# Kernel tuning notes

Measured on AMD Instinct MI355X. Metric: run time of the kernel, lower is better.

Reference implementation:

```python
import jax, jax.numpy as jnp
import numpy as np

N_USER, N_ITEM, D, K, E = 80000, 40000, 128, 10, 2000000

def _mlp(x, w1, b1, w2, b2, w3, b3):
    # MLP from source: linear->tanh->linear->tanh->linear->L2 normalize (eval mode, dropout off)
    x = jnp.tanh(x @ w1 + b1)
    x = jnp.tanh(x @ w2 + b2)
    x = x @ w3 + b3
    return x / jnp.maximum(jnp.linalg.norm(x, axis=-1, keepdims=True), 1e-12)

def setup_inputs() -> dict:
    key = jax.random.key(0)
    ks = jax.random.split(key, 24)
    s = 0.05
    inp = {
        'uemb_s': jax.random.normal(ks[0], (N_USER, D), jnp.float32),
        'iemb_s': jax.random.normal(ks[1], (N_ITEM, D), jnp.float32),
        'uemb_t': jax.random.normal(ks[2], (N_USER, D), jnp.float32),
        'u_emb_sp': jax.random.normal(ks[3], (N_USER, D), jnp.float32),
        'edge_user': jax.random.randint(ks[4], (E,), 0, N_USER, jnp.int32),
        'edge_item': jax.random.randint(ks[5], (E,), 0, N_ITEM, jnp.int32),
        # meta nets
        'Wu': jax.random.normal(ks[6], (4 * D, D), jnp.float32) * s,
        'bu': jnp.zeros((D,), jnp.float32),
        'Wi': jax.random.normal(ks[7], (2 * D, D), jnp.float32) * s,
        'bi': jnp.zeros((D,), jnp.float32),
        # mlp1: D -> D*K -> D//2 -> D*K
        'm1w1': jax.random.normal(ks[8], (D, D * K), jnp.float32) * s,
        'm1b1': jnp.zeros((D * K,), jnp.float32),
        'm1w2': jax.random.normal(ks[9], (D * K, D // 2), jnp.float32) * s,
        'm1b2': jnp.zeros((D // 2,), jnp.float32),
        'm1w3': jax.random.normal(ks[10], (D // 2, D * K), jnp.float32) * s,
        'm1b3': jnp.zeros((D * K,), jnp.float32),
        # mlp2: D -> D*K -> D//2 -> D*K
        'm2w1': jax.random.normal(ks[11], (D, D * K), jnp.float32) * s,
        'm2b1': jnp.zeros((D * K,), jnp.float32),
        'm2w2': jax.random.normal(ks[12], (D * K, D // 2), jnp.float32) * s,
        'm2b2': jnp.zeros((D // 2,), jnp.float32),
        'm2w3': jax.random.normal(ks[13], (D // 2, D * K), jnp.float32) * s,
        'm2b3': jnp.zeros((D * K,), jnp.float32),
    }
    return inp

def reference(uemb_s, iemb_s, uemb_t, u_emb_sp, edge_user, edge_item,
              Wu, bu, Wi, bi,
              m1w1, m1b1, m1w2, m1b2, m1w3, m1b3,
              m2w1, m2b1, m2w2, m2b2, m2w3, m2b3):
    # spmm with all-ones values == gather + segment_sum over the bipartite edge list
    neighbors_u = jax.ops.segment_sum(iemb_s[edge_item], edge_user, num_segments=N_USER)  # [U, D]
    tmp_embu = jax.lax.stop_gradient(
        jnp.concatenate([uemb_s, uemb_t, u_emb_sp, neighbors_u], axis=1)) @ Wu + bu       # [U, D]
    neighbors_i = jax.ops.segment_sum(((uemb_s + u_emb_sp) * 0.5)[edge_user], edge_item,
                                      num_segments=N_ITEM)                               # [I, D]
    tmp_embi = jax.lax.stop_gradient(
        jnp.concatenate([iemb_s, neighbors_i], axis=1)) @ Wi + bi                         # [I, D]
    metau = _mlp(tmp_embu, m1w1, m1b1, m1w2, m1b2, m1w3, m1b3).reshape(-1, D, K)          # [U, D, K]
    metai = _mlp(tmp_embi, m2w1, m2b1, m2w2, m2b2, m2w3, m2b3).reshape(-1, K, D)          # [I, K, D]
    meta_biasu = jnp.mean(metau, axis=0)  # [D, K]
    meta_biasi = jnp.mean(metai, axis=0)  # [K, D]
    low_weightu = jax.nn.softmax(metau + meta_biasu, axis=1)
    low_weighti = jax.nn.softmax(metai + meta_biasi, axis=1)
    return (low_weightu, low_weighti)
```

## Files before the change

### kernel.cpp

```cpp
#include <hip/hip_runtime.h>
#include <hip/hip_bf16.h>

#define D_ 128
#define DK_ 1280
#define K_ 10

typedef __attribute__((ext_vector_type(8))) short bh8;
typedef __attribute__((ext_vector_type(4))) short bh4;
typedef __attribute__((ext_vector_type(4))) float f32x4;

__device__ __forceinline__ short f2b(float f) {
    unsigned u = __builtin_bit_cast(unsigned, f);
    u += 0x7fffu + ((u >> 16) & 1u);
    return (short)(u >> 16);
}
__device__ __forceinline__ float b2f(short s) {
    unsigned u = ((unsigned)(unsigned short)s) << 16;
    return __builtin_bit_cast(float, u);
}
__device__ __forceinline__ float tanh_fast(float x) {
    float e = __expf(2.f * x);
    return 1.f - __fdividef(2.f, e + 1.f);
}
__device__ __forceinline__ f32x4 mfma16(bh8 a, bh8 b, f32x4 c) {
    return __builtin_amdgcn_mfma_f32_16x16x32_bf16(a, b, c, 0, 0, 0);
}

__device__ __forceinline__ int blk_excl_scan(int v, int t) {
    __shared__ int wp[4];
    int lane = t & 63, w = t >> 6;
    int s = v;
    for (int o = 1; o < 64; o <<= 1) {
        int pv = __shfl_up(s, o);
        if (lane >= o) s += pv;
    }
    if (lane == 63) wp[w] = s;
    __syncthreads();
    if (t == 0) {
        int a = 0;
#pragma unroll
        for (int k = 0; k < 4; ++k) { int x = wp[k]; wp[k] = a; a += x; }
    }
    __syncthreads();
    int r = s - v + wp[w];
    __syncthreads();
    return r;
}

__global__ __launch_bounds__(256) void cvt_all(
    const float* __restrict__ us, const float* __restrict__ ut,
    const float* __restrict__ usp, const float* __restrict__ is_,
    short* __restrict__ usb, short* __restrict__ utb,
    short* __restrict__ uspb, short* __restrict__ uavg, short* __restrict__ isb,
    int n4u, int n4i)
{
    int i = blockIdx.x * 256 + threadIdx.x;
    if (i < n4u) {
        float4 a = ((const float4*)us)[i];
        float4 b = ((const float4*)ut)[i];
        float4 c = ((const float4*)usp)[i];
        bh4 sa, sb, sc, sv;
        sa[0] = f2b(a.x); sa[1] = f2b(a.y); sa[2] = f2b(a.z); sa[3] = f2b(a.w);
        sb[0] = f2b(b.x); sb[1] = f2b(b.y); sb[2] = f2b(b.z); sb[3] = f2b(b.w);
        sc[0] = f2b(c.x); sc[1] = f2b(c.y); sc[2] = f2b(c.z); sc[3] = f2b(c.w);
        sv[0] = f2b(0.5f * (a.x + c.x)); sv[1] = f2b(0.5f * (a.y + c.y));
        sv[2] = f2b(0.5f * (a.z + c.z)); sv[3] = f2b(0.5f * (a.w + c.w));
        ((bh4*)usb)[i] = sa; ((bh4*)utb)[i] = sb;
        ((bh4*)uspb)[i] = sc; ((bh4*)uavg)[i] = sv;
    } else if (i < n4u + n4i) {
        int j = i - n4u;
        float4 v = ((const float4*)is_)[j];
        bh4 s;
        s[0] = f2b(v.x); s[1] = f2b(v.y); s[2] = f2b(v.z); s[3] = f2b(v.w);
        ((bh4*)isb)[j] = s;
    }
}

struct PackArgs {
    const float* W[8];
    short* o[8];
    int K[8];
    int N[8];
};
__global__ __launch_bounds__(256) void pack_all(PackArgs pa)
{
    int seg = blockIdx.y;
    int K = pa.K[seg], N = pa.N[seg];
    int total = K * N;
    int o = blockIdx.x * 256 + threadIdx.x;
    if (o >= total) return;
    const float* W = pa.W[seg];
    short* out = pa.o[seg];
    int j    = o & 7;
    int lane = (o >> 3) & 63;
    int rest = o >> 9;
    int KK = K >> 5;
    int kk = rest % KK;
    int tile = rest / KK;
    int k = kk * 32 + (lane >> 4) * 8 + j;
    int n = tile * 16 + (lane & 15);
    out[o] = f2b(W[(size_t)k * N + n]);
}

__global__ __launch_bounds__(256) void bhist_kernel(
    const int* __restrict__ eu, const int* __restrict__ ei,
    int* __restrict__ bcu, int* __restrict__ bci,
    int E, int shu, int shi, int nbu, int nbi)
{
    __shared__ int hu[160], hi[160];
    int t = threadIdx.x;
    int base = blockIdx.x * 4096;
    if (t < 160) { hu[t] = 0; hi[t] = 0; }
    __syncthreads();
    int n = min(4096, E - base);
#pragma unroll 4
    for (int k = 0; k < 16; ++k) {
        int idx = k * 256 + t;
        if (idx < n) {
            atomicAdd(&hu[eu[base + idx] >> shu], 1);
            atomicAdd(&hi[ei[base + idx] >> shi], 1);
        }
    }
    __syncthreads();
    if (t < nbu && hu[t]) atomicAdd(&bcu[t], hu[t]);
    if (t < nbi && hi[t]) atomicAdd(&bci[t], hi[t]);
}

__global__ __launch_bounds__(256) void binit_kernel(
    const int* __restrict__ bcu, int* __restrict__ gcu, int* __restrict__ bbu, int nbu,
    const int* __restrict__ bci, int* __restrict__ gci, int* __restrict__ bbi, int nbi,
    int E)
{
    int t = threadIdx.x;
    {
        int v = (t < nbu) ? bcu[t] : 0;
        int ex = blk_excl_scan(v, t);
        if (t < nbu) { gcu[t] = ex; bbu[t] = ex; }
        if (t == 0) bbu[nbu] = E;
    }
    __syncthreads();
    {
        int v = (t < nbi) ? bci[t] : 0;
        int ex = blk_excl_scan(v, t);
        if (t < nbi) { gci[t] = ex; bbi[t] = ex; }
        if (t == 0) bbi[nbi] = E;
    }
}

__global__ __launch_bounds__(256) void partition_kernel(
    const int* __restrict__ eu, const int* __restrict__ ei,
    int* __restrict__ gcu, int* __restrict__ gci,
    uint2* __restrict__ ebu, uint2* __restrict__ ebi,
    int E, int shu, int shi, int nbu, int nbi)
{
    __shared__ int hu[160], hi[160];
    int t = threadIdx.x;
    int base = blockIdx.x * 4096;
    if (t < 160) { hu[t] = 0; hi[t] = 0; }
    __syncthreads();
    int n = min(4096, E - base);
    int us[16], is_[16];
#pragma unroll 4
    for (int k = 0; k < 16; ++k) {
        int idx = k * 256 + t;
        if (idx < n) {
            us[k] = eu[base + idx];
            is_[k] = ei[base + idx];
            atomicAdd(&hu[us[k] >> shu], 1);
            atomicAdd(&hi[is_[k] >> shi], 1);
        } else us[k] = -1;
    }
    __syncthreads();
    if (t < nbu) { int c = hu[t]; hu[t] = c ? atomicAdd(&gcu[t], c) : 0; }
    if (t < nbi) { int c = hi[t]; hi[t] = c ? atomicAdd(&gci[t], c) : 0; }
    __syncthreads();
#pragma unroll 4
    for (int k = 0; k < 16; ++k) {
        if (us[k] >= 0) {
            int p1 = atomicAdd(&hu[us[k] >> shu], 1);
            ebu[p1] = make_uint2((unsigned)us[k], (unsigned)is_[k]);
            int p2 = atomicAdd(&hi[is_[k] >> shi], 1);
            ebi[p2] = make_uint2((unsigned)is_[k], (unsigned)us[k]);
        }
    }
}

__global__ __launch_bounds__(256) void fill2_all(
    const uint2* __restrict__ ebu, const int* __restrict__ bbu,
    int* __restrict__ off_u, int* __restrict__ end_u, int* __restrict__ adj_u,
    int NBU, int U,
    const uint2* __restrict__ ebi, const int* __restrict__ bbi,
    int* __restrict__ off_i, int* __restrict__ end_i, int* __restrict__ adj_i, int I)
{
    __shared__ int lcnt[512];
    __shared__ int lcur[512];
    bool isU = (int)blockIdx.x < NBU;
    const uint2* ebuf = isU ? ebu : ebi;
    const int* bbase  = isU ? bbu : bbi;
    int* off  = isU ? off_u : off_i;
    int* end_ = isU ? end_u : end_i;
    int* adj  = isU ? adj_u : adj_i;
    int span_sh = isU ? 9 : 8;
    int nrows = isU ? U : I;
    int b = isU ? blockIdx.x : blockIdx.x - NBU;

    int t = threadIdx.x;
    int rbase = b << span_sh;
    int span = min(1 << span_sh, nrows - rbase);
    int regbeg = bbase[b], regend = bbase[b + 1];
    for (int j = t; j < span; j += 256) lcnt[j] = 0;
    __syncthreads();
    for (int e = regbeg + t; e < regend; e += 256)
        atomicAdd(&lcnt[ebuf[e].x - rbase], 1);
    __syncthreads();
    int c0 = (2 * t < span) ? lcnt[2 * t] : 0;
    int c1 = (2 * t + 1 < span) ? lcnt[2 * t + 1] : 0;
    int ex = blk_excl_scan(c0 + c1, t);
    if (2 * t < span) {
        int beg = regbeg + ex;
        off[rbase + 2 * t] = beg;
        end_[rbase + 2 * t] = beg + c0;
        lcur[2 * t] = beg;
    }
    if (2 * t + 1 < span) {
        int beg = regbeg + ex + c0;
        off[rbase + 2 * t + 1] = beg;
        end_[rbase + 2 * t + 1] = beg + c1;
        lcur[2 * t + 1] = beg;
    }
    __syncthreads();
    for (int e = regbeg + t; e < regend; e += 256) {
        uint2 p = ebuf[e];
        int slot = atomicAdd(&lcur[p.x - rbase], 1);
        adj[slot] = (int)p.y;
    }
}

__global__ __launch_bounds__(256) void gather_all(
    const short* __restrict__ embU, const short* __restrict__ embI,
    const int* __restrict__ off_u, const int* __restrict__ end_u, const int* __restrict__ adj_u,
    const int* __restrict__ off_i, const int* __restrict__ end_i, const int* __restrict__ adj_i,
    short* __restrict__ nub, short* __restrict__ nib, int U, int I)
{
    int gw = (blockIdx.x * 256 + threadIdx.x) >> 6;
    int lane = threadIdx.x & 63;
    const short* emb; const int *offp, *endp, *adjp; short* outp; int row;
    if (gw < U)          { emb = embU; offp = off_u; endp = end_u; adjp = adj_u; outp = nub; row = gw; }
    else if (gw < U + I) { emb = embI; offp = off_i; endp = end_i; adjp = adj_i; outp = nib; row = gw - U; }
    else return;

    int beg = offp[row], end = endp[row];
    float ax = 0.f, ay = 0.f;
    int j = beg;
    for (; j + 3 < end; j += 4) {
        unsigned a = *(const unsigned*)(emb + (size_t)adjp[j]     * D_ + lane * 2);
        unsigned b = *(const unsigned*)(emb + (size_t)adjp[j + 1] * D_ + lane * 2);
        unsigned c = *(const unsigned*)(emb + (size_t)adjp[j + 2] * D_ + lane * 2);
        unsigned d = *(const unsigned*)(emb + (size_t)adjp[j + 3] * D_ + lane * 2);
        ax += b2f((short)(a & 0xffff)) + b2f((short)(b & 0xffff))
            + b2f((short)(c & 0xffff)) + b2f((short)(d & 0xffff));
        ay += b2f((short)(a >> 16)) + b2f((short)(b >> 16))
            + b2f((short)(c >> 16)) + b2f((short)(d >> 16));
    }
    for (; j < end; ++j) {
        unsigned a = *(const unsigned*)(emb + (size_t)adjp[j] * D_ + lane * 2);
        ax += b2f((short)(a & 0xffff));
        ay += b2f((short)(a >> 16));
    }
    unsigned o = ((unsigned)(unsigned short)f2b(ay) << 16) | (unsigned short)(unsigned)f2b(ax);
    *(unsigned*)(outp + (size_t)row * D_ + lane * 2) = o;
}

struct MlpArgs {
    const short *uA0, *uA1, *uA2, *uA3;
    const short *iA0, *iA1;
    const short *uWg, *uW1, *uW2, *uW3;
    const short *iWg, *iW1, *iW2, *iW3;
    const float *ubg, *ub1, *ub2, *ub3;
    const float *ibg, *ib1, *ib2, *ib3;
    short *uY, *iY;
    float *uNrm, *iNrm;
    int UB;
};

__global__ __launch_bounds__(256, 4) void fused_mlp_all(MlpArgs P)
{
    __shared__ char pool[35328];
    short* x2   = (short*)pool;
    short* h1q  = (short*)(pool + 8704);
    short* h2   = (short*)(pool + 29696);
    float* wred = (float*)(pool + 34304);

    const int t = threadIdx.x;
    const int l = t & 63;
    const int w = t >> 6;
    const int lr = l & 15;
    const int lg = l >> 4;

    const bool isU = (int)blockIdx.x < P.UB;
    const int bid = isU ? (int)blockIdx.x : (int)blockIdx.x - P.UB;
    const size_t rb0 = (size_t)bid * 32;
    const int KKG  = isU ? 16 : 8;
    const short* Wg = isU ? P.uWg : P.iWg;
    const short* W1 = isU ? P.uW1 : P.iW1;
    const short* W2 = isU ? P.uW2 : P.iW2;
    const short* W3 = isU ? P.uW3 : P.iW3;
    const float* bg = isU ? P.ubg : P.ibg;
    const float* b1 = isU ? P.ub1 : P.ib1;
    const float* b2 = isU ? P.ub2 : P.ib2;
    const float* b3 = isU ? P.ub3 : P.ib3;
    short* Ybf = isU ? P.uY : P.iY;
    float* Nrm = isU ? P.uNrm : P.iNrm;
    const short* srcs[4];
    if (isU) { srcs[0] = P.uA0; srcs[1] = P.uA1; srcs[2] = P.uA2; srcs[3] = P.uA3; }
    else     { srcs[0] = P.iA0; srcs[1] = P.iA1; srcs[2] = P.iA0; srcs[3] = P.iA1; }

    {
        f32x4 acc[2][2] = {{{0,0,0,0},{0,0,0,0}},{{0,0,0,0},{0,0,0,0}}};
        const short* wp = Wg + (size_t)(2 * w) * KKG * 512 + l * 8;
        const short* wq = wp + (size_t)KKG * 512;
        for (int kk = 0; kk < KKG; ++kk) {
            const short* src = srcs[kk >> 2];
            int coff = (kk & 3) * 32 + lg * 8;
            bh8 x0 = *(const bh8*)(src + (rb0 + lr) * D_ + coff);
            bh8 x1 = *(const bh8*)(src + (rb0 + 16 + lr) * D_ + coff);
            bh8 w0 = *(const bh8*)wp; wp += 512;
            bh8 w1 = *(const bh8*)wq; wq += 512;
            acc[0][0] = mfma16(w0, x0, acc[0][0]);
            acc[1][0] = mfma16(w0, x1, acc[1][0]);
            acc[0][1] = mfma16(w1, x0, acc[0][1]);
            acc[1][1] = mfma16(w1, x1, acc[1][1]);
        }
        float4 c0 = *(const float4*)(bg + (2 * w) * 16 + lg * 4);
        float4 c1 = *(const float4*)(bg + (2 * w + 1) * 16 + lg * 4);
#pragma unroll
        for (int rg = 0; rg < 2; ++rg) {
            bh4 p0, p1;
            p0[0] = f2b(acc[rg][0][0] + c0.x); p0[1] = f2b(acc[rg][0][1] + c0.y);
            p0[2] = f2b(acc[rg][0][2] + c0.z); p0[3] = f2b(acc[rg][0][3] + c0.w);
            p1[0] = f2b(acc[rg][1][0] + c1.x); p1[1] = f2b(acc[rg][1][1] + c1.y);
            p1[2] = f2b(acc[rg][1][2] + c1.z); p1[3] = f2b(acc[rg][1][3] + c1.w);
            *(bh4*)(x2 + (rg * 16 + lr) * 136 + (2 * w) * 16 + lg * 4) = p0;
            *(bh4*)(x2 + (rg * 16 + lr) * 136 + (2 * w + 1) * 16 + lg * 4) = p1;
        }
    }
    __syncthreads();

    bh8 xf[2][4];
#pragma unroll
    for (int rg = 0; rg < 2; ++rg)
#pragma unroll
        for (int kk = 0; kk < 4; ++kk)
            xf[rg][kk] = *(const bh8*)(x2 + (rg * 16 + lr) * 136 + kk * 32 + lg * 8);

    f32x4 c2[2][2] = {{{0,0,0,0},{0,0,0,0}},{{0,0,0,0},{0,0,0,0}}};
#pragma unroll 1
    for (int q = 0; q < 4; ++q) {
        const short* wp = W1 + (size_t)(q * 20 + w * 5) * 2048 + l * 8;
        const float* bp = b1 + (q * 20 + w * 5) * 16 + lg * 4;
#pragma unroll 1
        for (int tt = 0; tt < 5; ++tt) {
            f32x4 a0 = {0,0,0,0}, a1 = a0;
#pragma unroll
            for (int kk = 0; kk < 4; ++kk) {
                bh8 wf = *(const bh8*)wp; wp += 512;
                a0 = mfma16(wf, xf[0][kk], a0);
                a1 = mfma16(wf, xf[1][kk], a1);
            }
            float4 bv = *(const float4*)bp; bp += 16;
            bh4 pk0, pk1;
            pk0[0] = f2b(tanh_fast(a0[0] + bv.x)); pk0[1] = f2b(tanh_fast(a0[1] + bv.y));
            pk0[2] = f2b(tanh_fast(a0[2] + bv.z)); pk0[3] = f2b(tanh_fast(a0[3] + bv.w));
            pk1[0] = f2b(tanh_fast(a1[0] + bv.x)); pk1[1] = f2b(tanh_fast(a1[1] + bv.y));
            pk1[2] = f2b(tanh_fast(a1[2] + bv.z)); pk1[3] = f2b(tanh_fast(a1[3] + bv.w));
            int lt = w * 5 + tt;
            *(bh4*)(h1q + lr * 328 + lt * 16 + lg * 4) = pk0;
            *(bh4*)(h1q + (16 + lr) * 328 + lt * 16 + lg * 4) = pk1;
        }
        __syncthreads();
        const short* wp2 = W2 + (size_t)(w * 40 + q * 10) * 512 + l * 8;
        const short* hq0 = h1q + lr * 328 + lg * 8;
        const short* hq1 = h1q + (16 + lr) * 328 + lg * 8;
#pragma unroll 2
        for (int kk = 0; kk < 10; ++kk) {
            bh8 wf = *(const bh8*)wp2; wp2 += 512;
            bh8 h0 = *(const bh8*)(hq0 + kk * 32);
            bh8 h1v = *(const bh8*)(hq1 + kk * 32);
            if (kk & 1) { c2[0][1] = mfma16(wf, h0, c2[0][1]); c2[1][1] = mfma16(wf, h1v, c2[1][1]); }
            else        { c2[0][0] = mfma16(wf, h0, c2[0][0]); c2[1][0] = mfma16(wf, h1v, c2[1][0]); }
        }
        __syncthreads();
    }

    {
        float4 bv = *(const float4*)(b2 + w * 16 + lg * 4);
#pragma unroll
        for (int rg = 0; rg < 2; ++rg) {
            bh4 p2;
            p2[0] = f2b(tanh_fast(c2[rg][0][0] + c2[rg][1][0] + bv.x));
            p2[1] = f2b(tanh_fast(c2[rg][0][1] + c2[rg][1][1] + bv.y));
            p2[2] = f2b(tanh_fast(c2[rg][0][2] + c2[rg][1][2] + bv.z));
            p2[3] = f2b(tanh_fast(c2[rg][0][3] + c2[rg][1][3] + bv.w));
            *(bh4*)(h2 + (rg * 16 + lr) * 72 + w * 16 + lg * 4) = p2;
        }
    }
    __syncthreads();

    {
        bh8 hf[2][2];
#pragma unroll
        for (int rg = 0; rg < 2; ++rg) {
            hf[rg][0] = *(const bh8*)(h2 + (rg * 16 + lr) * 72 + lg * 8);
            hf[rg][1] = *(const bh8*)(h2 + (rg * 16 + lr) * 72 + 32 + lg * 8);
        }
        float ssq0 = 0.f, ssq1 = 0.f;
        const short* wp3 = W3 + (size_t)(w * 20) * 1024 + l * 8;
        const float* bp3 = b3 + w * 320 + lg * 4;
        short* dst0 = Ybf + (rb0 + lr) * DK_ + w * 320 + lg * 4;
        short* dst1 = Ybf + (rb0 + 16 + lr) * DK_ + w * 320 + lg * 4;
#pragma unroll 2
        for (int tt = 0; tt < 20; ++tt) {
            bh8 w0 = *(const bh8*)(wp3 + tt * 1024);
            bh8 w1 = *(const bh8*)(wp3 + tt * 1024 + 512);
            float4 bv = *(const float4*)(bp3 + tt * 16);
            f32x4 a0 = {0,0,0,0}, a1 = a0;
            a0 = mfma16(w0, hf[0][0], a0); a0 = mfma16(w1, hf[0][1], a0);
            a1 = mfma16(w0, hf[1][0], a1); a1 = mfma16(w1, hf[1][1], a1);
            float v00 = a0[0] + bv.x, v01 = a0[1] + bv.y, v02 = a0[2] + bv.z, v03 = a0[3] + bv.w;
            float v10 = a1[0] + bv.x, v11 = a1[1] + bv.y, v12 = a1[2] + bv.z, v13 = a1[3] + bv.w;
            ssq0 = fmaf(v00, v00, ssq0); ssq0 = fmaf(v01, v01, ssq0);
            ssq0 = fmaf(v02, v02, ssq0); ssq0 = fmaf(v03, v03, ssq0);
            ssq1 = fmaf(v10, v10, ssq1); ssq1 = fmaf(v11, v11, ssq1);
            ssq1 = fmaf(v12, v12, ssq1); ssq1 = fmaf(v13, v13, ssq1);
            bh4 o0, o1;
            o0[0] = f2b(v00); o0[1] = f2b(v01); o0[2] = f2b(v02); o0[3] = f2b(v03);
            o1[0] = f2b(v10); o1[1] = f2b(v11); o1[2] = f2b(v12); o1[3] = f2b(v13);
            *(bh4*)(dst0 + tt * 16) = o0;
            *(bh4*)(dst1 + tt * 16) = o1;
        }
        ssq0 += __shfl_xor(ssq0, 16); ssq0 += __shfl_xor(ssq0, 32);
        ssq1 += __shfl_xor(ssq1, 16); ssq1 += __shfl_xor(ssq1, 32);
        if (l < 16) {
            wred[w * 32 + l] = ssq0;
            wred[w * 32 + 16 + l] = ssq1;
        }
    }
    __syncthreads();
    if (t < 32) {
        float s = wred[t] + wred[32 + t] + wred[64 + t] + wred[96 + t];
        Nrm[rb0 + t] = 1.f / fmaxf(sqrtf(s), 1e-12f);
    }
}

__global__ __launch_bounds__(256) void finalize_bias(
    const short* __restrict__ Yu, const short* __restrict__ Yi,
    const float* __restrict__ nrmU, const float* __restrict__ nrmI,
    float* __restrict__ bsu, float* __restrict__ bsi, int U, int I, int NCH)
{
    int z = blockIdx.y;
    const short* Y = z ? Yi : Yu;
    const float* nr = z ? nrmI : nrmU;
    float* dst = z ? bsi : bsu;
    int M = z ? I : U;
    int chunk = (M + NCH - 1) / NCH;
    int r0 = blockIdx.x * chunk;
    int r1 = min(M, r0 + chunk);
    if (r0 >= r1) return;
    int t = threadIdx.x;
    float s0 = 0.f, s1 = 0.f, s2 = 0.f, s3 = 0.f, s4 = 0.f;
    for (int r = r0; r < r1; ++r) {
        const short* row = Y + (size_t)r * DK_;
        float nv = nr[r];
        s0 += b2f(row[t]) * nv;
        s1 += b2f(row[256 + t]) * nv;
        s2 += b2f(row[512 + t]) * nv;
        s3 += b2f(row[768 + t]) * nv;
        s4 += b2f(row[1024 + t]) * nv;
    }
    atomicAdd(&dst[t], s0);
    atomicAdd(&dst[256 + t], s1);
    atomicAdd(&dst[512 + t], s2);
    atomicAdd(&dst[768 + t], s3);
    atomicAdd(&dst[1024 + t], s4);
}

__global__ __launch_bounds__(64) void softmax_all(
    const short* __restrict__ Yu, const short* __restrict__ Yi,
    const float* __restrict__ nrmU, const float* __restrict__ nrmI,
    const float* __restrict__ bsu, const float* __restrict__ bsi,
    float invU, float invI,
    float* __restrict__ outu, float* __restrict__ outi, int U, int I)
{
    __shared__ float rowb[DK_];
    int b = blockIdx.x;
    int t = threadIdx.x;
    if (b < U) {
        size_t base = (size_t)b * DK_;
        float nrm = nrmU[b];
        for (int i = t; i < DK_ / 4; i += 64) {
            uint2 a = ((const uint2*)(Yu + base))[i];
            float4 bv = ((const float4*)bsu)[i];
            rowb[4 * i + 0] = b2f((short)(a.x & 0xffff)) * nrm + bv.x * invU;
            rowb[4 * i + 1] = b2f((short)(a.x >> 16))    * nrm + bv.y * invU;
            rowb[4 * i + 2] = b2f((short)(a.y & 0xffff)) * nrm + bv.z * invU;
            rowb[4 * i + 3] = b2f((short)(a.y >> 16))    * nrm + bv.w * invU;
        }
        __syncthreads();
#pragma unroll 1
        for (int k = 0; k < K_; ++k) {
            float v0 = rowb[t * K_ + k];
            float v1 = rowb[(t + 64) * K_ + k];
            float m = fmaxf(v0, v1);
            for (int off = 32; off; off >>= 1) m = fmaxf(m, __shfl_xor(m, off));
            float e0 = expf(v0 - m), e1 = expf(v1 - m);
            float s = e0 + e1;
            for (int off = 32; off; off >>= 1) s += __shfl_xor(s, off);
            float rs = 1.f / s;
            rowb[t * K_ + k] = e0 * rs;
            rowb[(t + 64) * K_ + k] = e1 * rs;
        }
        __syncthreads();
        for (int i = t; i < DK_ / 4; i += 64)
            ((float4*)(outu + base))[i] = ((const float4*)rowb)[i];
    } else {
        int it = b - U;
        if (it >= I) return;
        size_t base = (size_t)it * DK_;
        float nrm = nrmI[it];
        float v0[K_], v1[K_];
        float m0 = -1e30f, m1 = -1e30f;
#pragma unroll
        for (int k = 0; k < K_; ++k) {
            unsigned a = *(const unsigned*)(Yi + base + k * D_ + 2 * t);
            float2 bv = ((const float2*)(bsi + k * D_))[t];
            v0[k] = b2f((short)(a & 0xffff)) * nrm + bv.x * invI;
            v1[k] = b2f((short)(a >> 16))    * nrm + bv.y * invI;
            m0 = fmaxf(m0, v0[k]); m1 = fmaxf(m1, v1[k]);
        }
        float s0 = 0.f, s1 = 0.f;
#pragma unroll
        for (int k = 0; k < K_; ++k) {
            v0[k] = expf(v0[k] - m0); s0 += v0[k];
            v1[k] = expf(v1[k] - m1); s1 += v1[k];
        }
        float r0 = 1.f / s0, r1 = 1.f / s1;
#pragma unroll
        for (int k = 0; k < K_; ++k) {
            float2 o; o.x = v0[k] * r0; o.y = v1[k] * r1;
            ((float2*)(outi + base + k * D_))[t] = o;
        }
    }
}

extern "C" void kernel_launch(void* const* d_in, const int* in_sizes, int n_in,
                              void* d_out, int out_size, void* d_ws, size_t ws_size,
                              hipStream_t stream)
{
    const float* uemb_s   = (const float*)d_in[0];
    const float* iemb_s   = (const float*)d_in[1];
    const float* uemb_t   = (const float*)d_in[2];
    const float* u_emb_sp = (const float*)d_in[3];
    const int*   eu       = (const int*)d_in[4];
    const int*   ei       = (const int*)d_in[5];
    const float* Wu  = (const float*)d_in[6];
    const float* bu  = (const float*)d_in[7];
    const float* Wi  = (const float*)d_in[8];
    const float* bi  = (const float*)d_in[9];
    const float* m1w1 = (const float*)d_in[10];
    const float* m1b1 = (const float*)d_in[11];
    const float* m1w2 = (const float*)d_in[12];
    const float* m1b2 = (const float*)d_in[13];
    const float* m1w3 = (const float*)d_in[14];
    const float* m1b3 = (const float*)d_in[15];
    const float* m2w1 = (const float*)d_in[16];
    const float* m2b1 = (const float*)d_in[17];
    const float* m2w2 = (const float*)d_in[18];
    const float* m2b2 = (const float*)d_in[19];
    const float* m2w3 = (const float*)d_in[20];
    const float* m2b3 = (const float*)d_in[21];

    const int U = in_sizes[0] / D_;
    const int I = in_sizes[1] / D_;
    const int E = in_sizes[4];

    const int SHU = 9, SHI = 8;
    const int NBU = (U + 511) >> 9;
    const int NBI = (I + 255) >> 8;
    const int UB = U / 32, IB = I / 32;

    char* p = (char*)d_ws;
    auto alloc = [&](size_t bytes) { char* r = p; p += (bytes + 255) & ~(size_t)255; return r; };

    short* usb  = (short*)alloc((size_t)U * D_ * 2);
    short* utb  = (short*)alloc((size_t)U * D_ * 2);
    short* uspb = (short*)alloc((size_t)U * D_ * 2);
    short* uavg = (short*)alloc((size_t)U * D_ * 2);
    short* isb  = (short*)alloc((size_t)I * D_ * 2);
    short* nub  = (short*)alloc((size_t)U * D_ * 2);
    short* nib  = (short*)alloc((size_t)I * D_ * 2);
    short* ybu  = (short*)alloc((size_t)U * DK_ * 2);
    short* ybi  = (short*)alloc((size_t)I * DK_ * 2);
    float* nrmU = (float*)alloc((size_t)U * 4);
    float* nrmI = (float*)alloc((size_t)I * 4);
    short* WgU  = (short*)alloc(512 * 128 * 2);
    short* WgI  = (short*)alloc(256 * 128 * 2);
    short* W1U  = (short*)alloc(128 * 1280 * 2);
    short* W2U  = (short*)alloc(1280 * 64 * 2);
    short* W3U  = (short*)alloc(64 * 1280 * 2);
    short* W1I  = (short*)alloc(128 * 1280 * 2);
    short* W2I  = (short*)alloc(1280 * 64 * 2);
    short* W3I  = (short*)alloc(64 * 1280 * 2);
    int*   zbuf = (int*)alloc((320 + 2 * DK_) * 4);
    int* bcnt_u = zbuf;
    int* bcnt_i = zbuf + 160;
    float* bsu  = (float*)(zbuf + 320);
    float* bsi  = bsu + DK_;
    int* gcur_u = (int*)alloc(160 * 4);
    int* gcur_i = (int*)alloc(160 * 4);
    int* bbase_u = (int*)alloc(161 * 4);
    int* bbase_i = (int*)alloc(161 * 4);
    int* off_u  = (int*)alloc((size_t)U * 4);
    int* end_u  = (int*)alloc((size_t)U * 4);
    int* off_i  = (int*)alloc((size_t)I * 4);
    int* end_i  = (int*)alloc((size_t)I * 4);
    uint2* ebu  = (uint2*)alloc((size_t)E * 8);
    uint2* ebi  = (uint2*)alloc((size_t)E * 8);
    int* adj_u  = (int*)alloc((size_t)E * 4);
    int* adj_i  = (int*)alloc((size_t)E * 4);

    float* outu = (float*)d_out;
    float* outi = outu + (size_t)U * DK_;

    hipMemsetAsync(zbuf, 0, (320 + 2 * DK_) * 4, stream);

    int n4u = U * D_ / 4, n4i = I * D_ / 4;
    cvt_all<<<(n4u + n4i + 255) / 256, 256, 0, stream>>>(
        uemb_s, uemb_t, u_emb_sp, iemb_s, usb, utb, uspb, uavg, isb, n4u, n4i);

    PackArgs pa;
    pa.W[0] = Wu;   pa.o[0] = WgU; pa.K[0] = 512;  pa.N[0] = 128;
    pa.W[1] = Wi;   pa.o[1] = WgI; pa.K[1] = 256;  pa.N[1] = 128;
    pa.W[2] = m1w1; pa.o[2] = W1U; pa.K[2] = 128;  pa.N[2] = 1280;
    pa.W[3] = m1w2; pa.o[3] = W2U; pa.K[3] = 1280; pa.N[3] = 64;
    pa.W[4] = m1w3; pa.o[4] = W3U; pa.K[4] = 64;   pa.N[4] = 1280;
    pa.W[5] = m2w1; pa.o[5] = W1I; pa.K[5] = 128;  pa.N[5] = 1280;
    pa.W[6] = m2w2; pa.o[6] = W2I; pa.K[6] = 1280; pa.N[6] = 64;
    pa.W[7] = m2w3; pa.o[7] = W3I; pa.K[7] = 64;   pa.N[7] = 1280;
    pack_all<<<dim3(640, 8), 256, 0, stream>>>(pa);

    int pb = (E + 4095) / 4096;
    bhist_kernel<<<pb, 256, 0, stream>>>(eu, ei, bcnt_u, bcnt_i, E, SHU, SHI, NBU, NBI);
    binit_kernel<<<1, 256, 0, stream>>>(bcnt_u, gcur_u, bbase_u, NBU,
                                        bcnt_i, gcur_i, bbase_i, NBI, E);
    partition_kernel<<<pb, 256, 0, stream>>>(eu, ei, gcur_u, gcur_i, ebu, ebi,
                                             E, SHU, SHI, NBU, NBI);
    fill2_all<<<NBU + NBI, 256, 0, stream>>>(ebu, bbase_u, off_u, end_u, adj_u, NBU, U,
                                             ebi, bbase_i, off_i, end_i, adj_i, I);

    gather_all<<<(U + I + 3) / 4, 256, 0, stream>>>(
        isb, uavg, off_u, end_u, adj_u, off_i, end_i, adj_i, nub, nib, U, I);

    MlpArgs ma;
    ma.uA0 = usb; ma.uA1 = utb; ma.uA2 = uspb; ma.uA3 = nub;
    ma.iA0 = isb; ma.iA1 = nib;
    ma.uWg = WgU; ma.uW1 = W1U; ma.uW2 = W2U; ma.uW3 = W3U;
    ma.iWg = WgI; ma.iW1 = W1I; ma.iW2 = W2I; ma.iW3 = W3I;
    ma.ubg = bu; ma.ub1 = m1b1; ma.ub2 = m1b2; ma.ub3 = m1b3;
    ma.ibg = bi; ma.ib1 = m2b1; ma.ib2 = m2b2; ma.ib3 = m2b3;
    ma.uY = ybu; ma.iY = ybi;
    ma.uNrm = nrmU; ma.iNrm = nrmI;
    ma.UB = UB;
    fused_mlp_all<<<UB + IB, 256, 0, stream>>>(ma);

    finalize_bias<<<dim3(256, 2), 256, 0, stream>>>(ybu, ybi, nrmU, nrmI, bsu, bsi, U, I, 256);

    softmax_all<<<U + I, 64, 0, stream>>>(ybu, ybi, nrmU, nrmI, bsu, bsi,
                                          1.0f / (float)U, 1.0f / (float)I, outu, outi, U, I);
}
```

Baseline: 929.4 us.

## Split fused MLP into two per-wave passes and pack edge buffers to 32-bit

The fused block-wide MLP kernel is replaced by two kernels in which each wave handles a 32-row job on its own. Pass 1 computes the meta linear layer and the first hidden layer and writes the 1280-wide tanh activations to global memory. Pass 2 reads them back and computes the second and third layers, the output and the norm. This removes block-level __syncthreads and the shared h1 staging, at the cost of an extra round trip of 1280 bf16 values per row through global memory. Separately, the partitioned edge records are packed into one 32-bit word (local row offset plus neighbour index) instead of a uint2, which halves that buffer's traffic.

Result: slower. 1.133 ms (+21.9%).

```diff
diff --git a/kernel.cpp b/kernel.cpp
--- a/kernel.cpp
+++ b/kernel.cpp
@@ -150,7 +150,7 @@
 __global__ __launch_bounds__(256) void partition_kernel(
     const int* __restrict__ eu, const int* __restrict__ ei,
     int* __restrict__ gcu, int* __restrict__ gci,
-    uint2* __restrict__ ebu, uint2* __restrict__ ebi,
+    unsigned* __restrict__ ebu, unsigned* __restrict__ ebi,
     int E, int shu, int shi, int nbu, int nbi)
 {
     __shared__ int hu[160], hi[160];
@@ -178,29 +178,31 @@
     for (int k = 0; k < 16; ++k) {
         if (us[k] >= 0) {
             int p1 = atomicAdd(&hu[us[k] >> shu], 1);
-            ebu[p1] = make_uint2((unsigned)us[k], (unsigned)is_[k]);
+            ebu[p1] = ((unsigned)(us[k] & 511) << 16) | (unsigned)is_[k];
             int p2 = atomicAdd(&hi[is_[k] >> shi], 1);
-            ebi[p2] = make_uint2((unsigned)is_[k], (unsigned)us[k]);
+            ebi[p2] = ((unsigned)(is_[k] & 255) << 17) | (unsigned)us[k];
         }
     }
 }
 
 __global__ __launch_bounds__(256) void fill2_all(
-    const uint2* __restrict__ ebu, const int* __restrict__ bbu,
+    const unsigned* __restrict__ ebu, const int* __restrict__ bbu,
     int* __restrict__ off_u, int* __restrict__ end_u, int* __restrict__ adj_u,
     int NBU, int U,
-    const uint2* __restrict__ ebi, const int* __restrict__ bbi,
+    const unsigned* __restrict__ ebi, const int* __restrict__ bbi,
     int* __restrict__ off_i, int* __restrict__ end_i, int* __restrict__ adj_i, int I)
 {
     __shared__ int lcnt[512];
     __shared__ int lcur[512];
     bool isU = (int)blockIdx.x < NBU;
-    const uint2* ebuf = isU ? ebu : ebi;
+    const unsigned* ebuf = isU ? ebu : ebi;
     const int* bbase  = isU ? bbu : bbi;
     int* off  = isU ? off_u : off_i;
     int* end_ = isU ? end_u : end_i;
     int* adj  = isU ? adj_u : adj_i;
     int span_sh = isU ? 9 : 8;
+    int pay_sh = isU ? 16 : 17;
+    unsigned pmask = (1u << pay_sh) - 1u;
     int nrows = isU ? U : I;
     int b = isU ? blockIdx.x : blockIdx.x - NBU;
 
@@ -211,7 +213,7 @@
     for (int j = t; j < span; j += 256) lcnt[j] = 0;
     __syncthreads();
     for (int e = regbeg + t; e < regend; e += 256)
-        atomicAdd(&lcnt[ebuf[e].x - rbase], 1);
+        atomicAdd(&lcnt[ebuf[e] >> pay_sh], 1);
     __syncthreads();
     int c0 = (2 * t < span) ? lcnt[2 * t] : 0;
     int c1 = (2 * t + 1 < span) ? lcnt[2 * t + 1] : 0;
@@ -230,9 +232,9 @@
     }
     __syncthreads();
     for (int e = regbeg + t; e < regend; e += 256) {
-        uint2 p = ebuf[e];
-        int slot = atomicAdd(&lcur[p.x - rbase], 1);
-        adj[slot] = (int)p.y;
+        unsigned p = ebuf[e];
+        int slot = atomicAdd(&lcur[p >> pay_sh], 1);
+        adj[slot] = (int)(p & pmask);
     }
 }
 
@@ -271,80 +273,69 @@
     *(unsigned*)(outp + (size_t)row * D_ + lane * 2) = o;
 }
 
-struct MlpArgs {
+struct P1Args {
     const short *uA0, *uA1, *uA2, *uA3;
     const short *iA0, *iA1;
-    const short *uWg, *uW1, *uW2, *uW3;
-    const short *iWg, *iW1, *iW2, *iW3;
-    const float *ubg, *ub1, *ub2, *ub3;
-    const float *ibg, *ib1, *ib2, *ib3;
-    short *uY, *iY;
-    float *uNrm, *iNrm;
-    int UB;
+    const short *uWg, *uW1;
+    const short *iWg, *iW1;
+    const float *ubg, *ub1;
+    const float *ibg, *ib1;
+    short *uH, *iH;
+    int UJ, TOT;
 };
 
-__global__ __launch_bounds__(256, 4) void fused_mlp_all(MlpArgs P)
-{
-    __shared__ char pool[35328];
-    short* x2   = (short*)pool;
-    short* h1q  = (short*)(pool + 8704);
-    short* h2   = (short*)(pool + 29696);
-    float* wred = (float*)(pool + 34304);
-
+__global__ __launch_bounds__(256, 4) void mlp_pass1(P1Args P)
+{
+    __shared__ short x2s[4][32 * 136];
     const int t = threadIdx.x;
     const int l = t & 63;
     const int w = t >> 6;
     const int lr = l & 15;
     const int lg = l >> 4;
-
-    const bool isU = (int)blockIdx.x < P.UB;
-    const int bid = isU ? (int)blockIdx.x : (int)blockIdx.x - P.UB;
+    short* x2 = x2s[w];
+
+    int job = blockIdx.x * 4 + w;
+    if (job >= P.TOT) return;
+    const bool isU = job < P.UJ;
+    const int bid = isU ? job : job - P.UJ;
     const size_t rb0 = (size_t)bid * 32;
-    const int KKG  = isU ? 16 : 8;
+    const int KKG = isU ? 16 : 8;
     const short* Wg = isU ? P.uWg : P.iWg;
     const short* W1 = isU ? P.uW1 : P.iW1;
-    const short* W2 = isU ? P.uW2 : P.iW2;
-    const short* W3 = isU ? P.uW3 : P.iW3;
     const float* bg = isU ? P.ubg : P.ibg;
     const float* b1 = isU ? P.ub1 : P.ib1;
-    const float* b2 = isU ? P.ub2 : P.ib2;
-    const float* b3 = isU ? P.ub3 : P.ib3;
-    short* Ybf = isU ? P.uY : P.iY;
-    float* Nrm = isU ? P.uNrm : P.iNrm;
+    short* H = isU ? P.uH : P.iH;
     const short* srcs[4];
     if (isU) { srcs[0] = P.uA0; srcs[1] = P.uA1; srcs[2] = P.uA2; srcs[3] = P.uA3; }
     else     { srcs[0] = P.iA0; srcs[1] = P.iA1; srcs[2] = P.iA0; srcs[3] = P.iA1; }
 
-    {
+#pragma unroll 1
+    for (int p = 0; p < 4; ++p) {
         f32x4 acc[2][2] = {{{0,0,0,0},{0,0,0,0}},{{0,0,0,0},{0,0,0,0}}};
-        const short* wp = Wg + (size_t)(2 * w) * KKG * 512 + l * 8;
-        const short* wq = wp + (size_t)KKG * 512;
         for (int kk = 0; kk < KKG; ++kk) {
             const short* src = srcs[kk >> 2];
             int coff = (kk & 3) * 32 + lg * 8;
             bh8 x0 = *(const bh8*)(src + (rb0 + lr) * D_ + coff);
             bh8 x1 = *(const bh8*)(src + (rb0 + 16 + lr) * D_ + coff);
-            bh8 w0 = *(const bh8*)wp; wp += 512;
-            bh8 w1 = *(const bh8*)wq; wq += 512;
+            bh8 w0 = *(const bh8*)(Wg + ((size_t)(2 * p) * KKG + kk) * 512 + l * 8);
+            bh8 w1 = *(const bh8*)(Wg + ((size_t)(2 * p + 1) * KKG + kk) * 512 + l * 8);
             acc[0][0] = mfma16(w0, x0, acc[0][0]);
             acc[1][0] = mfma16(w0, x1, acc[1][0]);
             acc[0][1] = mfma16(w1, x0, acc[0][1]);
             acc[1][1] = mfma16(w1, x1, acc[1][1]);
         }
-        float4 c0 = *(const float4*)(bg + (2 * w) * 16 + lg * 4);
-        float4 c1 = *(const float4*)(bg + (2 * w + 1) * 16 + lg * 4);
-#pragma unroll
-        for (int rg = 0; rg < 2; ++rg) {
-            bh4 p0, p1;
-            p0[0] = f2b(acc[rg][0][0] + c0.x); p0[1] = f2b(acc[rg][0][1] + c0.y);
-            p0[2] = f2b(acc[rg][0][2] + c0.z); p0[3] = f2b(acc[rg][0][3] + c0.w);
-            p1[0] = f2b(acc[rg][1][0] + c1.x); p1[1] = f2b(acc[rg][1][1] + c1.y);
-            p1[2] = f2b(acc[rg][1][2] + c1.z); p1[3] = f2b(acc[rg][1][3] + c1.w);
-            *(bh4*)(x2 + (rg * 16 + lr) * 136 + (2 * w) * 16 + lg * 4) = p0;
-            *(bh4*)(x2 + (rg * 16 + lr) * 136 + (2 * w + 1) * 16 + lg * 4) = p1;
-        }
-    }
-    __syncthreads();
+#pragma unroll
+        for (int q = 0; q < 2; ++q) {
+            float4 bv = *(const float4*)(bg + (2 * p + q) * 16 + lg * 4);
+#pragma unroll
+            for (int rg = 0; rg < 2; ++rg) {
+                bh4 pk;
+                pk[0] = f2b(acc[rg][q][0] + bv.x); pk[1] = f2b(acc[rg][q][1] + bv.y);
+                pk[2] = f2b(acc[rg][q][2] + bv.z); pk[3] = f2b(acc[rg][q][3] + bv.w);
+                *(bh4*)(x2 + (rg * 16 + lr) * 136 + (2 * p + q) * 16 + lg * 4) = pk;
+            }
+        }
+    }
 
     bh8 xf[2][4];
 #pragma unroll
@@ -353,102 +344,121 @@
         for (int kk = 0; kk < 4; ++kk)
             xf[rg][kk] = *(const bh8*)(x2 + (rg * 16 + lr) * 136 + kk * 32 + lg * 8);
 
-    f32x4 c2[2][2] = {{{0,0,0,0},{0,0,0,0}},{{0,0,0,0},{0,0,0,0}}};
-#pragma unroll 1
-    for (int q = 0; q < 4; ++q) {
-        const short* wp = W1 + (size_t)(q * 20 + w * 5) * 2048 + l * 8;
-        const float* bp = b1 + (q * 20 + w * 5) * 16 + lg * 4;
-#pragma unroll 1
-        for (int tt = 0; tt < 5; ++tt) {
-            f32x4 a0 = {0,0,0,0}, a1 = a0;
-#pragma unroll
-            for (int kk = 0; kk < 4; ++kk) {
-                bh8 wf = *(const bh8*)wp; wp += 512;
-                a0 = mfma16(wf, xf[0][kk], a0);
-                a1 = mfma16(wf, xf[1][kk], a1);
-            }
-            float4 bv = *(const float4*)bp; bp += 16;
-            bh4 pk0, pk1;
-            pk0[0] = f2b(tanh_fast(a0[0] + bv.x)); pk0[1] = f2b(tanh_fast(a0[1] + bv.y));
-            pk0[2] = f2b(tanh_fast(a0[2] + bv.z)); pk0[3] = f2b(tanh_fast(a0[3] + bv.w));
-            pk1[0] = f2b(tanh_fast(a1[0] + bv.x)); pk1[1] = f2b(tanh_fast(a1[1] + bv.y));
-            pk1[2] = f2b(tanh_fast(a1[2] + bv.z)); pk1[3] = f2b(tanh_fast(a1[3] + bv.w));
-            int lt = w * 5 + tt;
-            *(bh4*)(h1q + lr * 328 + lt * 16 + lg * 4) = pk0;
-            *(bh4*)(h1q + (16 + lr) * 328 + lt * 16 + lg * 4) = pk1;
-        }
-        __syncthreads();
-        const short* wp2 = W2 + (size_t)(w * 40 + q * 10) * 512 + l * 8;
-        const short* hq0 = h1q + lr * 328 + lg * 8;
-        const short* hq1 = h1q + (16 + lr) * 328 + lg * 8;
 #pragma unroll 2
-        for (int kk = 0; kk < 10; ++kk) {
-            bh8 wf = *(const bh8*)wp2; wp2 += 512;
-            bh8 h0 = *(const bh8*)(hq0 + kk * 32);
-            bh8 h1v = *(const bh8*)(hq1 + kk * 32);
-            if (kk & 1) { c2[0][1] = mfma16(wf, h0, c2[0][1]); c2[1][1] = mfma16(wf, h1v, c2[1][1]); }
-            else        { c2[0][0] = mfma16(wf, h0, c2[0][0]); c2[1][0] = mfma16(wf, h1v, c2[1][0]); }
-        }
-        __syncthreads();
-    }
-
-    {
-        float4 bv = *(const float4*)(b2 + w * 16 + lg * 4);
+    for (int gt = 0; gt < 80; ++gt) {
+        const short* wp = W1 + (size_t)gt * 2048 + l * 8;
+        f32x4 a0 = {0,0,0,0}, a1 = a0;
+#pragma unroll
+        for (int kk = 0; kk < 4; ++kk) {
+            bh8 wf = *(const bh8*)(wp + kk * 512);
+            a0 = mfma16(wf, xf[0][kk], a0);
+            a1 = mfma16(wf, xf[1][kk], a1);
+        }
+        float4 bv = *(const float4*)(b1 + gt * 16 + lg * 4);
+        bh4 p0, p1;
+        p0[0] = f2b(tanh_fast(a0[0] + bv.x)); p0[1] = f2b(tanh_fast(a0[1] + bv.y));
+        p0[2] = f2b(tanh_fast(a0[2] + bv.z)); p0[3] = f2b(tanh_fast(a0[3] + bv.w));
+        p1[0] = f2b(tanh_fast(a1[0] + bv.x)); p1[1] = f2b(tanh_fast(a1[1] + bv.y));
+        p1[2] = f2b(tanh_fast(a1[2] + bv.z)); p1[3] = f2b(tanh_fast(a1[3] + bv.w));
+        *(bh4*)(H + (rb0 + lr) * DK_ + gt * 16 + lg * 4) = p0;
+        *(bh4*)(H + (rb0 + 16 + lr) * DK_ + gt * 16 + lg * 4) = p1;
+    }
+}
+
+struct P2Args {
+    const short *uW2, *uW3;
+    const short *iW2, *iW3;
+    const float *ub2, *ub3;
+    const float *ib2, *ib3;
+    short *uH, *iH;
+    float *uNrm, *iNrm;
+    int UJ, TOT;
+};
+
+__global__ __launch_bounds__(256, 3) void mlp_pass2(P2Args P)
+{
+    __shared__ short h2s[4][32 * 72];
+    const int t = threadIdx.x;
+    const int l = t & 63;
+    const int w = t >> 6;
+    const int lr = l & 15;
+    const int lg = l >> 4;
+    short* h2 = h2s[w];
+
+    int job = blockIdx.x * 4 + w;
+    if (job >= P.TOT) return;
+    const bool isU = job < P.UJ;
+    const int bid = isU ? job : job - P.UJ;
+    const size_t rb0 = (size_t)bid * 32;
+    const short* W2 = isU ? P.uW2 : P.iW2;
+    const short* W3 = isU ? P.uW3 : P.iW3;
+    const float* b2 = isU ? P.ub2 : P.ib2;
+    const float* b3 = isU ? P.ub3 : P.ib3;
+    short* H = isU ? P.uH : P.iH;
+    float* Nrm = isU ? P.uNrm : P.iNrm;
+
+    f32x4 c2[2][4] = {{{0,0,0,0},{0,0,0,0},{0,0,0,0},{0,0,0,0}},
+                      {{0,0,0,0},{0,0,0,0},{0,0,0,0},{0,0,0,0}}};
+#pragma unroll 2
+    for (int kk = 0; kk < 40; ++kk) {
+        bh8 h0 = *(const bh8*)(H + (rb0 + lr) * DK_ + kk * 32 + lg * 8);
+        bh8 h1v = *(const bh8*)(H + (rb0 + 16 + lr) * DK_ + kk * 32 + lg * 8);
+        const short* wp2 = W2 + (size_t)kk * 512 + l * 8;
+#pragma unroll
+        for (int tile = 0; tile < 4; ++tile) {
+            bh8 wf = *(const bh8*)(wp2 + (size_t)tile * 40 * 512);
+            c2[0][tile] = mfma16(wf, h0, c2[0][tile]);
+            c2[1][tile] = mfma16(wf, h1v, c2[1][tile]);
+        }
+    }
+
+#pragma unroll
+    for (int tile = 0; tile < 4; ++tile) {
+        float4 bv = *(const float4*)(b2 + tile * 16 + lg * 4);
 #pragma unroll
         for (int rg = 0; rg < 2; ++rg) {
             bh4 p2;
-            p2[0] = f2b(tanh_fast(c2[rg][0][0] + c2[rg][1][0] + bv.x));
-            p2[1] = f2b(tanh_fast(c2[rg][0][1] + c2[rg][1][1] + bv.y));
-            p2[2] = f2b(tanh_fast(c2[rg][0][2] + c2[rg][1][2] + bv.z));
-            p2[3] = f2b(tanh_fast(c2[rg][0][3] + c2[rg][1][3] + bv.w));
-            *(bh4*)(h2 + (rg * 16 + lr) * 72 + w * 16 + lg * 4) = p2;
-        }
-    }
-    __syncthreads();
-
-    {
-        bh8 hf[2][2];
-#pragma unroll
-        for (int rg = 0; rg < 2; ++rg) {
-            hf[rg][0] = *(const bh8*)(h2 + (rg * 16 + lr) * 72 + lg * 8);
-            hf[rg][1] = *(const bh8*)(h2 + (rg * 16 + lr) * 72 + 32 + lg * 8);
-        }
-        float ssq0 = 0.f, ssq1 = 0.f;
-        const short* wp3 = W3 + (size_t)(w * 20) * 1024 + l * 8;
-        const float* bp3 = b3 + w * 320 + lg * 4;
-        short* dst0 = Ybf + (rb0 + lr) * DK_ + w * 320 + lg * 4;
-        short* dst1 = Ybf + (rb0 + 16 + lr) * DK_ + w * 320 + lg * 4;
+            p2[0] = f2b(tanh_fast(c2[rg][tile][0] + bv.x));
+            p2[1] = f2b(tanh_fast(c2[rg][tile][1] + bv.y));
+            p2[2] = f2b(tanh_fast(c2[rg][tile][2] + bv.z));
+            p2[3] = f2b(tanh_fast(c2[rg][tile][3] + bv.w));
+            *(bh4*)(h2 + (rg * 16 + lr) * 72 + tile * 16 + lg * 4) = p2;
+        }
+    }
+
+    bh8 hf[2][2];
+#pragma unroll
+    for (int rg = 0; rg < 2; ++rg) {
+        hf[rg][0] = *(const bh8*)(h2 + (rg * 16 + lr) * 72 + lg * 8);
+        hf[rg][1] = *(const bh8*)(h2 + (rg * 16 + lr) * 72 + 32 + lg * 8);
+    }
+    float ssq0 = 0.f, ssq1 = 0.f;
 #pragma unroll 2
-        for (int tt = 0; tt < 20; ++tt) {
-            bh8 w0 = *(const bh8*)(wp3 + tt * 1024);
-            bh8 w1 = *(const bh8*)(wp3 + tt * 1024 + 512);
-            float4 bv = *(const float4*)(bp3 + tt * 16);
-            f32x4 a0 = {0,0,0,0}, a1 = a0;
-            a0 = mfma16(w0, hf[0][0], a0); a0 = mfma16(w1, hf[0][1], a0);
-            a1 = mfma16(w0, hf[1][0], a1); a1 = mfma16(w1, hf[1][1], a1);
-            float v00 = a0[0] + bv.x, v01 = a0[1] + bv.y, v02 = a0[2] + bv.z, v03 = a0[3] + bv.w;
-            float v10 = a1[0] + bv.x, v11 = a1[1] + bv.y, v12 = a1[2] + bv.z, v13 = a1[3] + bv.w;
-            ssq0 = fmaf(v00, v00, ssq0); ssq0 = fmaf(v01, v01, ssq0);
-            ssq0 = fmaf(v02, v02, ssq0); ssq0 = fmaf(v03, v03, ssq0);
-            ssq1 = fmaf(v10, v10, ssq1); ssq1 = fmaf(v11, v11, ssq1);
-            ssq1 = fmaf(v12, v12, ssq1); ssq1 = fmaf(v13, v13, ssq1);
-            bh4 o0, o1;
-            o0[0] = f2b(v00); o0[1] = f2b(v01); o0[2] = f2b(v02); o0[3] = f2b(v03);
-            o1[0] = f2b(v10); o1[1] = f2b(v11); o1[2] = f2b(v12); o1[3] = f2b(v13);
-            *(bh4*)(dst0 + tt * 16) = o0;
-            *(bh4*)(dst1 + tt * 16) = o1;
-        }
-        ssq0 += __shfl_xor(ssq0, 16); ssq0 += __shfl_xor(ssq0, 32);
-        ssq1 += __shfl_xor(ssq1, 16); ssq1 += __shfl_xor(ssq1, 32);
-        if (l < 16) {
-            wred[w * 32 + l] = ssq0;
-            wred[w * 32 + 16 + l] = ssq1;
-        }
-    }
-    __syncthreads();
-    if (t < 32) {
-        float s = wred[t] + wred[32 + t] + wred[64 + t] + wred[96 + t];
-        Nrm[rb0 + t] = 1.f / fmaxf(sqrtf(s), 1e-12f);
+    for (int tt = 0; tt < 80; ++tt) {
+        const short* wp3 = W3 + (size_t)tt * 1024 + l * 8;
+        bh8 w0 = *(const bh8*)wp3;
+        bh8 w1 = *(const bh8*)(wp3 + 512);
+        float4 bv = *(const float4*)(b3 + tt * 16 + lg * 4);
+        f32x4 a0 = {0,0,0,0}, a1 = a0;
+        a0 = mfma16(w0, hf[0][0], a0); a0 = mfma16(w1, hf[0][1], a0);
+        a1 = mfma16(w0, hf[1][0], a1); a1 = mfma16(w1, hf[1][1], a1);
+        float v00 = a0[0] + bv.x, v01 = a0[1] + bv.y, v02 = a0[2] + bv.z, v03 = a0[3] + bv.w;
+        float v10 = a1[0] + bv.x, v11 = a1[1] + bv.y, v12 = a1[2] + bv.z, v13 = a1[3] + bv.w;
+        ssq0 = fmaf(v00, v00, ssq0); ssq0 = fmaf(v01, v01, ssq0);
+        ssq0 = fmaf(v02, v02, ssq0); ssq0 = fmaf(v03, v03, ssq0);
+        ssq1 = fmaf(v10, v10, ssq1); ssq1 = fmaf(v11, v11, ssq1);
+        ssq1 = fmaf(v12, v12, ssq1); ssq1 = fmaf(v13, v13, ssq1);
+        bh4 o0, o1;
+        o0[0] = f2b(v00); o0[1] = f2b(v01); o0[2] = f2b(v02); o0[3] = f2b(v03);
+        o1[0] = f2b(v10); o1[1] = f2b(v11); o1[2] = f2b(v12); o1[3] = f2b(v13);
+        *(bh4*)(H + (rb0 + lr) * DK_ + tt * 16 + lg * 4) = o0;
+        *(bh4*)(H + (rb0 + 16 + lr) * DK_ + tt * 16 + lg * 4) = o1;
+    }
+    ssq0 += __shfl_xor(ssq0, 16); ssq0 += __shfl_xor(ssq0, 32);
+    ssq1 += __shfl_xor(ssq1, 16); ssq1 += __shfl_xor(ssq1, 32);
+    if (l < 16) {
+        Nrm[rb0 + l] = 1.f / fmaxf(sqrtf(ssq0), 1e-12f);
+        Nrm[rb0 + 16 + l] = 1.f / fmaxf(sqrtf(ssq1), 1e-12f);
     }
 }
 
@@ -586,7 +596,8 @@
     const int SHU = 9, SHI = 8;
     const int NBU = (U + 511) >> 9;
     const int NBI = (I + 255) >> 8;
-    const int UB = U / 32, IB = I / 32;
+    const int UJ = U / 32, IJ = I / 32;
+    const int TOT = UJ + IJ;
 
     char* p = (char*)d_ws;
     auto alloc = [&](size_t bytes) { char* r = p; p += (bytes + 255) & ~(size_t)255; return r; };
@@ -623,8 +634,8 @@
     int* end_u  = (int*)alloc((size_t)U * 4);
     int* off_i  = (int*)alloc((size_t)I * 4);
     int* end_i  = (int*)alloc((size_t)I * 4);
-    uint2* ebu  = (uint2*)alloc((size_t)E * 8);
-    uint2* ebi  = (uint2*)alloc((size_t)E * 8);
+    unsigned* ebu = (unsigned*)alloc((size_t)E * 4);
+    unsigned* ebi = (unsigned*)alloc((size_t)E * 4);
     int* adj_u  = (int*)alloc((size_t)E * 4);
     int* adj_i  = (int*)alloc((size_t)E * 4);
 
@@ -660,17 +671,26 @@
     gather_all<<<(U + I + 3) / 4, 256, 0, stream>>>(
         isb, uavg, off_u, end_u, adj_u, off_i, end_i, adj_i, nub, nib, U, I);
 
-    MlpArgs ma;
-    ma.uA0 = usb; ma.uA1 = utb; ma.uA2 = uspb; ma.uA3 = nub;
-    ma.iA0 = isb; ma.iA1 = nib;
-    ma.uWg = WgU; ma.uW1 = W1U; ma.uW2 = W2U; ma.uW3 = W3U;
-    ma.iWg = WgI; ma.iW1 = W1I; ma.iW2 = W2I; ma.iW3 = W3I;
-    ma.ubg = bu; ma.ub1 = m1b1; ma.ub2 = m1b2; ma.ub3 = m1b3;
-    ma.ibg = bi; ma.ib1 = m2b1; ma.ib2 = m2b2; ma.ib3 = m2b3;
-    ma.uY = ybu; ma.iY = ybi;
-    ma.uNrm = nrmU; ma.iNrm = nrmI;
-    ma.UB = UB;
-    fused_mlp_all<<<UB + IB, 256, 0, stream>>>(ma);
+    P1Args p1;
+    p1.uA0 = usb; p1.uA1 = utb; p1.uA2 = uspb; p1.uA3 = nub;
+    p1.iA0 = isb; p1.iA1 = nib;
+    p1.uWg = WgU; p1.uW1 = W1U;
+    p1.iWg = WgI; p1.iW1 = W1I;
+    p1.ubg = bu;  p1.ub1 = m1b1;
+    p1.ibg = bi;  p1.ib1 = m2b1;
+    p1.uH = ybu;  p1.iH = ybi;
+    p1.UJ = UJ;   p1.TOT = TOT;
+    mlp_pass1<<<(TOT + 3) / 4, 256, 0, stream>>>(p1);
+
+    P2Args p2;
+    p2.uW2 = W2U; p2.uW3 = W3U;
+    p2.iW2 = W2I; p2.iW3 = W3I;
+    p2.ub2 = m1b2; p2.ub3 = m1b3;
+    p2.ib2 = m2b2; p2.ib3 = m2b3;
+    p2.uH = ybu;  p2.iH = ybi;
+    p2.uNrm = nrmU; p2.iNrm = nrmI;
+    p2.UJ = UJ;   p2.TOT = TOT;
+    mlp_pass2<<<(TOT + 3) / 4, 256, 0, stream>>>(p2);
 
     finalize_bias<<<dim3(256, 2), 256, 0, stream>>>(ybu, ybi, nrmU, nrmI, bsu, bsi, U, I, 256);
 
```
